# Kernel tuning notes

Hardware: AMD Instinct MI355X
Metric: run time of the kernel (lower is better)

The kernel has to match this reference:

```python
import jax, jax.numpy as jnp
import numpy as np

B, T, V, E, H, K = 64, 1024, 50000, 128, 256, 20
HD = H // 2  # hidden per LSTM direction


def _p(key, i, shape, scale=0.05):
    return jax.random.normal(jax.random.fold_in(key, i), shape, dtype=jnp.float32) * scale


def setup_inputs():
    key = jax.random.key(0)
    k1, k2, k3 = jax.random.split(key, 3)
    lengths = jax.random.randint(k2, (B,), T // 4, T + 1)
    mask = jnp.arange(T)[None, :] < lengths[:, None]  # [B,T] bool, left-aligned
    x = jax.random.randint(k1, (B, T), 1, V)
    x = jnp.where(mask, x, 0).astype(jnp.int32)  # pad_idx = 0
    tags = jax.random.randint(k3, (B, T), 0, K).astype(jnp.int32)
    inp = {"x": x, "tags": tags, "mask": mask}
    pk = jax.random.key(1)
    inp["emb"] = _p(pk, 0, (V, E)).at[0].set(0.0)  # padding_idx row zeroed
    dims = [E, H]  # layer-1 input is concat of both directions = H
    i = 1
    for l in range(2):
        for suf in ["", "_rev"]:
            inp[f"w_ih_l{l}{suf}"] = _p(pk, i, (4 * HD, dims[l])); i += 1
            inp[f"w_hh_l{l}{suf}"] = _p(pk, i, (4 * HD, HD)); i += 1
            inp[f"b_ih_l{l}{suf}"] = _p(pk, i, (4 * HD,)); i += 1
            inp[f"b_hh_l{l}{suf}"] = _p(pk, i, (4 * HD,)); i += 1
    inp["ln_g"] = jnp.ones((H,), jnp.float32)
    inp["ln_b"] = jnp.zeros((H,), jnp.float32)
    inp["attn_w"] = _p(pk, i, (1, H)); i += 1
    inp["attn_b"] = _p(pk, i, (1,)); i += 1
    inp["fc1_w"] = _p(pk, i, (H, H)); i += 1
    inp["fc1_b"] = _p(pk, i, (H,)); i += 1
    inp["fc2_w"] = _p(pk, i, (K, H)); i += 1
    inp["fc2_b"] = _p(pk, i, (K,)); i += 1
    inp["crf_start"] = _p(pk, i, (K,)); i += 1
    inp["crf_end"] = _p(pk, i, (K,)); i += 1
    inp["crf_trans"] = _p(pk, i, (K, K)); i += 1
    return inp


def _lstm_dir(x, w_ih, w_hh, b_ih, b_hh, reverse):
    # x: [B,T,D] -> [B,T,HD]; torch gate order i,f,g,o
    xs = jnp.swapaxes(x, 0, 1)  # [T,B,D]
    pre = xs @ w_ih.T + b_ih + b_hh  # input contribution precomputed (GEMM)

    def step(carry, g_in):
        h, c = carry
        g = g_in + h @ w_hh.T
        i, f, gc, o = jnp.split(g, 4, axis=-1)
        c = jax.nn.sigmoid(f) * c + jax.nn.sigmoid(i) * jnp.tanh(gc)
        h = jax.nn.sigmoid(o) * jnp.tanh(c)
        return (h, c), h

    nB, nH = x.shape[0], w_hh.shape[1]
    init = (jnp.zeros((nB, nH), x.dtype), jnp.zeros((nB, nH), x.dtype))
    _, hs = jax.lax.scan(step, init, pre, reverse=reverse)
    return jnp.swapaxes(hs, 0, 1)


def _crf_nll(emissions, tags, mask, start, end, trans):
    # torchcrf: llh = score - logZ, reduction='sum'; module returns -llh.mean() (scalar)
    maskf = mask.astype(emissions.dtype)
    em_sc = jnp.take_along_axis(emissions, tags[..., None], axis=2)[..., 0]  # [B,T]
    tr_sc = trans[tags[:, :-1], tags[:, 1:]]  # [B,T-1]
    num = start[tags[:, 0]] + em_sc[:, 0] + jnp.sum(maskf[:, 1:] * (tr_sc + em_sc[:, 1:]), axis=1)
    last = jnp.sum(mask.astype(jnp.int32), axis=1) - 1
    last_tags = jnp.take_along_axis(tags, last[:, None], axis=1)[:, 0]
    num = num + end[last_tags]
    alpha0 = start[None, :] + emissions[:, 0]  # [B,K]
    em_t = jnp.swapaxes(emissions[:, 1:], 0, 1)  # [T-1,B,K]
    m_t = jnp.swapaxes(mask[:, 1:], 0, 1)  # [T-1,B]

    def step(alpha, inp):
        e, m = inp
        nxt = jax.scipy.special.logsumexp(alpha[:, :, None] + trans[None] + e[:, None, :], axis=1)
        return jnp.where(m[:, None], nxt, alpha), None

    alpha, _ = jax.lax.scan(step, alpha0, (em_t, m_t))
    logZ = jax.scipy.special.logsumexp(alpha + end[None, :], axis=1)
    return -jnp.sum(num - logZ)


def reference(x, tags, mask, emb,
              w_ih_l0, w_hh_l0, b_ih_l0, b_hh_l0,
              w_ih_l0_rev, w_hh_l0_rev, b_ih_l0_rev, b_hh_l0_rev,
              w_ih_l1, w_hh_l1, b_ih_l1, b_hh_l1,
              w_ih_l1_rev, w_hh_l1_rev, b_ih_l1_rev, b_hh_l1_rev,
              ln_g, ln_b, attn_w, attn_b, fc1_w, fc1_b, fc2_w, fc2_b,
              crf_start, crf_end, crf_trans):
    mask = mask.at[:, 0].set(True)
    h = emb[x]  # [B,T,E]
    # 2-layer bidirectional LSTM (eval mode: dropout = identity)
    h = jnp.concatenate([
        _lstm_dir(h, w_ih_l0, w_hh_l0, b_ih_l0, b_hh_l0, False),
        _lstm_dir(h, w_ih_l0_rev, w_hh_l0_rev, b_ih_l0_rev, b_hh_l0_rev, True)], axis=-1)
    h = jnp.concatenate([
        _lstm_dir(h, w_ih_l1, w_hh_l1, b_ih_l1, b_hh_l1, False),
        _lstm_dir(h, w_ih_l1_rev, w_hh_l1_rev, b_ih_l1_rev, b_hh_l1_rev, True)], axis=-1)
    # LayerNorm (eps=1e-5)
    mu = jnp.mean(h, axis=-1, keepdims=True)
    var = jnp.mean(jnp.square(h - mu), axis=-1, keepdims=True)
    h = (h - mu) * jax.lax.rsqrt(var + 1e-5) * ln_g + ln_b
    # masked attention + residual broadcast of context
    scores = (h @ attn_w.T)[..., 0] + attn_b[0]  # [B,T]
    scores = jnp.where(mask, scores, jnp.float32(-1e9))
    w = jax.nn.softmax(scores, axis=1)[..., None]  # [B,T,1]
    h = h + jnp.sum(h * w, axis=1, keepdims=True)
    # hidden_fc: Linear + ReLU (dropout identity in eval)
    h = jax.nn.relu(h @ fc1_w.T + fc1_b)
    emissions = h @ fc2_w.T + fc2_b  # [B,T,K]
    return _crf_nll(emissions, tags, mask, crf_start, crf_end, crf_trans)
```

## Files before the change

kernel.cpp:

```cpp
#include <hip/hip_runtime.h>
#include <stdint.h>

#define BB 64
#define TT 1024
#define EE 128

typedef __bf16 bf16x8 __attribute__((ext_vector_type(8)));
typedef float f32x4 __attribute__((ext_vector_type(4)));

#define MFMA16 __builtin_amdgcn_mfma_f32_16x16x32_bf16

__device__ __forceinline__ float bf2f(unsigned short u) {
  union { unsigned int i; float f; } v; v.i = ((unsigned int)u) << 16; return v.f;
}
__device__ __forceinline__ unsigned short f2bf(float f) {
  union { float f; unsigned int i; } v; v.f = f;
  return (unsigned short)((v.i + 0x7fffu + ((v.i >> 16) & 1u)) >> 16);
}
__device__ __forceinline__ float sigf(float x) {
  return __builtin_amdgcn_rcpf(1.f + __expf(-x));
}
__device__ __forceinline__ float tanhf_(float x) {
  return fmaf(2.f, __builtin_amdgcn_rcpf(1.f + __expf(-2.f * x)), -1.f);
}


__global__ __launch_bounds__(256) void cvtbf4(const float* __restrict__ s,
                                              unsigned short* __restrict__ d, int n4) {
  int i = blockIdx.x * 256 + threadIdx.x;
  if (i < n4) {
    float4 v = *(const float4*)&s[(size_t)i * 4];
    ushort4 o; o.x = f2bf(v.x); o.y = f2bf(v.y); o.z = f2bf(v.z); o.w = f2bf(v.w);
    *(ushort4*)&d[(size_t)i * 4] = o;
  }
}

__global__ __launch_bounds__(256) void bias_comb(const float* bi, const float* bh,
                                                 const float* bir, const float* bhr,
                                                 float* __restrict__ o) {
  int j = blockIdx.x * 256 + threadIdx.x;
  if (j < 1024) o[j] = (j < 512) ? (bi[j] + bh[j]) : (bir[j - 512] + bhr[j - 512]);
}

__global__ __launch_bounds__(256) void embed_k(const int* __restrict__ x,
                                               const float* __restrict__ emb,
                                               unsigned short* __restrict__ xe) {
  int i = blockIdx.x * 256 + threadIdx.x;
  int bt = i >> 5, e4 = (i & 31) << 2;
  float4 v = *(const float4*)&emb[(size_t)x[bt] * EE + e4];
  ushort4 o; o.x = f2bf(v.x); o.y = f2bf(v.y); o.z = f2bf(v.z); o.w = f2bf(v.w);
  *(ushort4*)&xe[(size_t)bt * EE + e4] = o;
}


template <bool RELU, bool REMAP>
__global__ __launch_bounds__(256) void gemm_bt(const unsigned short* __restrict__ A,
                                               const unsigned short* __restrict__ W,
                                               const float* __restrict__ bias,
                                               unsigned short* __restrict__ out,
                                               int M, int N, int K) {
  __shared__ unsigned short As[64][40];
  __shared__ unsigned short Ws[64][40];
  __shared__ unsigned short Cs[64][72];
  const int tid = threadIdx.x, wave = tid >> 6, lane = tid & 63;
  const int m0 = blockIdx.x * 64, n0 = blockIdx.y * 64;
  f32x4 acc[4] = {{0,0,0,0},{0,0,0,0},{0,0,0,0},{0,0,0,0}};
  const int r = tid >> 2, kc = (tid & 3) << 3;
  const int fr = lane & 15, kk = (lane >> 4) << 3;

  for (int k0 = 0; k0 < K; k0 += 32) {
    uint4 av = *(const uint4*)&A[(size_t)(m0 + r) * K + k0 + kc];
    uint4 wv = *(const uint4*)&W[(size_t)(n0 + r) * K + k0 + kc];
    *(uint4*)&As[r][kc] = av;
    *(uint4*)&Ws[r][kc] = wv;
    __syncthreads();
    bf16x8 af = *(const bf16x8*)&As[wave * 16 + fr][kk];
#pragma unroll
    for (int nt = 0; nt < 4; nt++) {
      bf16x8 bv = *(const bf16x8*)&Ws[nt * 16 + fr][kk];
      acc[nt] = MFMA16(af, bv, acc[nt], 0, 0, 0);
    }
    __syncthreads();
  }
  const int cr = (lane >> 4) << 2, cc = lane & 15;
#pragma unroll
  for (int nt = 0; nt < 4; nt++) {
    float bs = bias[n0 + nt * 16 + cc];
#pragma unroll
    for (int rr = 0; rr < 4; rr++) {
      float v = acc[nt][rr] + bs;
      if (RELU) v = fmaxf(v, 0.f);
      Cs[wave * 16 + cr + rr][nt * 16 + cc] = f2bf(v);
    }
  }
  __syncthreads();
  const int row = tid >> 2, c0 = (tid & 3) * 16;
  uint4 v0 = *(const uint4*)&Cs[row][c0];
  uint4 v1 = *(const uint4*)&Cs[row][c0 + 8];
  const int gm = m0 + row;
  size_t off;
  if (REMAP) { int b = gm >> 10, t = gm & 1023; off = ((size_t)(t * 64 + b)) * N + n0 + c0; }
  else       { off = (size_t)gm * N + n0 + c0; }
  *(uint4*)&out[off] = v0;
  *(uint4*)&out[off + 8] = v1;
}


#define SCAN_STEP10(PG0, PG1, PG2, PG3, TIDX) {                               \
    bf16x8 bv0 = *(const bf16x8*)&hS[p][q * 8];                               \
    bf16x8 bv1 = *(const bf16x8*)&hS[p][32 + q * 8];                          \
    bf16x8 bv2 = *(const bf16x8*)&hS[p][64 + q * 8];                          \
    bf16x8 bv3 = *(const bf16x8*)&hS[p][96 + q * 8];                          \
    f32x4 c0 = {0,0,0,0}, c1 = {0,0,0,0}, c2 = {0,0,0,0}, c3 = {0,0,0,0};     \
    c0 = MFMA16(bv0, af[0][0], c0, 0,0,0); c1 = MFMA16(bv0, af[1][0], c1, 0,0,0); \
    c2 = MFMA16(bv0, af[2][0], c2, 0,0,0); c3 = MFMA16(bv0, af[3][0], c3, 0,0,0); \
    c0 = MFMA16(bv1, af[0][1], c0, 0,0,0); c1 = MFMA16(bv1, af[1][1], c1, 0,0,0); \
    c2 = MFMA16(bv1, af[2][1], c2, 0,0,0); c3 = MFMA16(bv1, af[3][1], c3, 0,0,0); \
    c0 = MFMA16(bv2, af[0][2], c0, 0,0,0); c1 = MFMA16(bv2, af[1][2], c1, 0,0,0); \
    c2 = MFMA16(bv2, af[2][2], c2, 0,0,0); c3 = MFMA16(bv2, af[3][2], c3, 0,0,0); \
    c0 = MFMA16(bv3, af[0][3], c0, 0,0,0); c1 = MFMA16(bv3, af[1][3], c1, 0,0,0); \
    c2 = MFMA16(bv3, af[2][3], c2, 0,0,0); c3 = MFMA16(bv3, af[3][3], c3, 0,0,0); \
    float gi = c0[0] + bf2f(PG0);                                             \
    float gf = c1[0] + bf2f(PG1);                                             \
    float gg = c2[0] + bf2f(PG2);                                             \
    float go = c3[0] + bf2f(PG3);                                             \
    float cn = sigf(gf) * c + sigf(gi) * tanhf_(gg);                          \
    c = cn;                                                                   \
    float h = sigf(go) * tanhf_(cn);                                          \
    unsigned short hb_ = f2bf(h);                                             \
    if (q == 0) {                                                             \
      hS[p ^ 1][u] = hb_;                                                     \
      hob[(size_t)(TIDX) * 256] = hb_;                   \
    }                                                                         \
  }

__global__ __launch_bounds__(512) void lstm_scan10(const unsigned short* __restrict__ pre,
                                                   const unsigned short* __restrict__ whhb,
                                                   unsigned short* __restrict__ hout) {
  const int b = blockIdx.x, dir = blockIdx.y;
  const int tid = threadIdx.x;
  const int w = tid >> 6, lane = tid & 63;
  const int fr = lane & 15, q = lane >> 4;
  const int u = 16 * w + fr;
  const unsigned short* wb = whhb + (size_t)dir * 65536;

  bf16x8 af[4][4];
#pragma unroll
  for (int G = 0; G < 4; G++)
#pragma unroll
    for (int kt = 0; kt < 4; kt++)
      af[G][kt] = *(const bf16x8*)&wb[(size_t)(128 * G + 16 * w + fr) * 128 + kt * 32 + q * 8];
  asm volatile("" : "+v"(af[0][0]), "+v"(af[0][1]), "+v"(af[0][2]), "+v"(af[0][3]),
                    "+v"(af[1][0]), "+v"(af[1][1]), "+v"(af[1][2]), "+v"(af[1][3]),
                    "+v"(af[2][0]), "+v"(af[2][1]), "+v"(af[2][2]), "+v"(af[2][3]),
                    "+v"(af[3][0]), "+v"(af[3][1]), "+v"(af[3][2]), "+v"(af[3][3]));

  __shared__ alignas(16) unsigned short hS[2][128];
  if (tid < 128) { hS[0][tid] = 0; hS[1][tid] = 0; }

  const int t0 = dir ? 1023 : 0, st = dir ? -1 : 1;
  float c = 0.f;
  const unsigned short* pb = pre + (size_t)b * 1024 + dir * 512 + u;
  unsigned short* hob = hout + (size_t)b * 1024 * 256 + dir * 128 + u;

  unsigned short pA0, pA1, pA2, pA3, pB0, pB1, pB2, pB3;
  {
    size_t tb = (size_t)t0 * 65536;
    pA0 = pb[tb]; pA1 = pb[tb + 128]; pA2 = pb[tb + 256]; pA3 = pb[tb + 384];
    tb = (size_t)(t0 + st) * 65536;
    pB0 = pb[tb]; pB1 = pb[tb + 128]; pB2 = pb[tb + 256]; pB3 = pb[tb + 384];
  }
  __syncthreads();

  int p = 0;
  for (int s = 0; s < 1024; s += 2) {
    const int t = t0 + st * s;
    SCAN_STEP10(pA0, pA1, pA2, pA3, t)
    if (s + 2 < 1024) {
      size_t tb = (size_t)(t0 + st * (s + 2)) * 65536;
      pA0 = pb[tb]; pA1 = pb[tb + 128]; pA2 = pb[tb + 256]; pA3 = pb[tb + 384];
    }
    asm volatile("s_waitcnt lgkmcnt(0)\n\ts_barrier" ::: "memory");
    p ^= 1;
    SCAN_STEP10(pB0, pB1, pB2, pB3, t + st)
    if (s + 3 < 1024) {
      size_t tb = (size_t)(t0 + st * (s + 3)) * 65536;
      pB0 = pb[tb]; pB1 = pb[tb + 128]; pB2 = pb[tb + 256]; pB3 = pb[tb + 384];
    }
    asm volatile("s_waitcnt lgkmcnt(0)\n\ts_barrier" ::: "memory");
    p ^= 1;
  }
}


__global__ __launch_bounds__(256) void ln_attn(const unsigned short* __restrict__ h,
                                               const float* __restrict__ g,
                                               const float* __restrict__ be,
                                               const float* __restrict__ aw,
                                               const float* __restrict__ ab,
                                               unsigned short* __restrict__ hln,
                                               float* __restrict__ sc) {
  int row = blockIdx.x * 4 + (threadIdx.x >> 6);
  int lane = threadIdx.x & 63;
  ushort4 u = *(const ushort4*)&h[(size_t)row * 256 + lane * 4];
  float vx = bf2f(u.x), vy = bf2f(u.y), vz = bf2f(u.z), vw = bf2f(u.w);
  float s = vx + vy + vz + vw;
#pragma unroll
  for (int o = 1; o < 64; o <<= 1) s += __shfl_xor(s, o);
  float mu = s * (1.f / 256.f);
  float dx = vx - mu, dy = vy - mu, dz = vz - mu, dw = vw - mu;
  float q = dx * dx + dy * dy + dz * dz + dw * dw;
#pragma unroll
  for (int o = 1; o < 64; o <<= 1) q += __shfl_xor(q, o);
  float inv = rsqrtf(q * (1.f / 256.f) + 1e-5f);
  float4 gg = *(const float4*)&g[lane * 4];
  float4 bb = *(const float4*)&be[lane * 4];
  float y0 = dx * inv * gg.x + bb.x;
  float y1 = dy * inv * gg.y + bb.y;
  float y2 = dz * inv * gg.z + bb.z;
  float y3 = dw * inv * gg.w + bb.w;
  ushort4 ov; ov.x = f2bf(y0); ov.y = f2bf(y1); ov.z = f2bf(y2); ov.w = f2bf(y3);
  *(ushort4*)&hln[(size_t)row * 256 + lane * 4] = ov;
  float4 av = *(const float4*)&aw[lane * 4];
  float p = y0 * av.x + y1 * av.y + y2 * av.z + y3 * av.w;
#pragma unroll
  for (int o = 1; o < 64; o <<= 1) p += __shfl_xor(p, o);
  if (lane == 0) sc[row] = p + ab[0];
}


__global__ __launch_bounds__(256) void attn_pool(const float* __restrict__ scores,
                                                 const int* __restrict__ x,
                                                 const unsigned short* __restrict__ h_ln,
                                                 float* __restrict__ pooled) {
  int b = blockIdx.x, tid = threadIdx.x;
  __shared__ float wls[1024];
  __shared__ float red[4];
  float mx = -1e30f;
  for (int t = tid; t < 1024; t += 256) {
    bool valid = (t == 0) || (x[b * 1024 + t] != 0);
    float s = valid ? scores[b * 1024 + t] : -1e9f;
    wls[t] = s;
    mx = fmaxf(mx, s);
  }
#pragma unroll
  for (int o = 1; o < 64; o <<= 1) mx = fmaxf(mx, __shfl_xor(mx, o));
  if ((tid & 63) == 0) red[tid >> 6] = mx;
  __syncthreads();
  mx = fmaxf(fmaxf(red[0], red[1]), fmaxf(red[2], red[3]));
  __syncthreads();
  float sm = 0.f;
  for (int t = tid; t < 1024; t += 256) {
    float e = __expf(wls[t] - mx);
    wls[t] = e;
    sm += e;
  }
#pragma unroll
  for (int o = 1; o < 64; o <<= 1) sm += __shfl_xor(sm, o);
  if ((tid & 63) == 0) red[tid >> 6] = sm;
  __syncthreads();
  sm = red[0] + red[1] + red[2] + red[3];
  float inv = 1.f / sm;
  float a0 = 0.f, a1 = 0.f, a2 = 0.f, a3 = 0.f;
  const unsigned short* hb = h_ln + (size_t)b * 1024 * 256 + tid;
  for (int t = 0; t < 1024; t += 4) {
    a0 = fmaf(wls[t + 0], bf2f(hb[(size_t)(t + 0) * 256]), a0);
    a1 = fmaf(wls[t + 1], bf2f(hb[(size_t)(t + 1) * 256]), a1);
    a2 = fmaf(wls[t + 2], bf2f(hb[(size_t)(t + 2) * 256]), a2);
    a3 = fmaf(wls[t + 3], bf2f(hb[(size_t)(t + 3) * 256]), a3);
  }
  pooled[b * 256 + tid] = ((a0 + a1) + (a2 + a3)) * inv;
}

__global__ __launch_bounds__(256) void h2add(const unsigned short* __restrict__ h_ln,
                                             const float* __restrict__ pooled,
                                             unsigned short* __restrict__ h2) {
  size_t i = ((size_t)blockIdx.x * 256 + threadIdx.x) * 4;
  int b = (int)(i >> 18);
  int cidx = (int)(i & 255);
  ushort4 v = *(const ushort4*)&h_ln[i];
  float4 p = *(const float4*)&pooled[b * 256 + cidx];
  ushort4 o;
  o.x = f2bf(bf2f(v.x) + p.x); o.y = f2bf(bf2f(v.y) + p.y);
  o.z = f2bf(bf2f(v.z) + p.z); o.w = f2bf(bf2f(v.w) + p.w);
  *(ushort4*)&h2[i] = o;
}


__global__ __launch_bounds__(256) void fc2_emis(const unsigned short* __restrict__ fin,
                                                const float* __restrict__ w,
                                                const float* __restrict__ bias,
                                                float* __restrict__ em) {
  int row = blockIdx.x * 4 + (threadIdx.x >> 6);
  int lane = threadIdx.x & 63;
  ushort4 u = *(const ushort4*)&fin[(size_t)row * 256 + lane * 4];
  float x0 = bf2f(u.x), x1 = bf2f(u.y), x2 = bf2f(u.z), x3 = bf2f(u.w);
  float acc[20];
#pragma unroll
  for (int jj = 0; jj < 20; jj++) {
    float4 wv = *(const float4*)&w[jj * 256 + lane * 4];
    acc[jj] = x0 * wv.x + x1 * wv.y + x2 * wv.z + x3 * wv.w;
  }
#pragma unroll
  for (int jj = 0; jj < 20; jj++) {
#pragma unroll
    for (int o = 1; o < 64; o <<= 1) acc[jj] += __shfl_xor(acc[jj], o);
  }
  if (lane == 0) {
#pragma unroll
    for (int jj = 0; jj < 20; jj++) em[(size_t)row * 20 + jj] = acc[jj] + bias[jj];
  }
}


__global__ __launch_bounds__(64) void crf_k(const float* __restrict__ em,
                                            const int* __restrict__ tags,
                                            const int* __restrict__ x,
                                            const float* __restrict__ cs,
                                            const float* __restrict__ ce,
                                            const float* __restrict__ ctr,
                                            float* __restrict__ part) {
  int b = blockIdx.x, lane = threadIdx.x;
  const float* eb = em + (size_t)b * 1024 * 20;
  const int* tb = tags + b * 1024;
  const int* xb = x + b * 1024;

  int cnt = 0;
  for (int t = lane; t < 1024; t += 64) cnt += (t == 0 || xb[t] != 0) ? 1 : 0;
#pragma unroll
  for (int o = 1; o < 64; o <<= 1) cnt += __shfl_xor(cnt, o);
  int len = cnt;

  float ns = 0.f;
  for (int t = 1 + lane; t < len; t += 64)
    ns += ctr[tb[t - 1] * 20 + tb[t]] + eb[(size_t)t * 20 + tb[t]];
#pragma unroll
  for (int o = 1; o < 64; o <<= 1) ns += __shfl_xor(ns, o);
  float num = ns + cs[tb[0]] + eb[tb[0]] + ce[tb[len - 1]];

  __shared__ float al[32];
  if (lane < 32) al[lane] = (lane < 20) ? (cs[lane] + eb[lane]) : -1e30f;
  __syncthreads();

  int p = lane / 20, jj = lane % 20;
  int i0 = p * 7;
  float trc[7];
#pragma unroll
  for (int i = 0; i < 7; i++)
    trc[i] = (i0 + i < 20) ? ctr[(i0 + i) * 20 + jj] : -1e30f;

  for (int t = 1; t < len; t++) {
    float aa[7];
    float m = -3e30f;
#pragma unroll
    for (int i = 0; i < 7; i++) {
      float a = ((i0 + i < 28) ? al[i0 + i] : -1e30f) + trc[i];
      aa[i] = a;
      m = fmaxf(m, a);
    }
    float m0 = __shfl(m, jj), m1 = __shfl(m, jj + 20), m2 = __shfl(m, jj + 40);
    float mj = fmaxf(fmaxf(m0, m1), m2);
    float s = 0.f;
#pragma unroll
    for (int i = 0; i < 7; i++) s += __expf(aa[i] - mj);
    float s0 = __shfl(s, jj), s1 = __shfl(s, jj + 20), s2 = __shfl(s, jj + 40);
    float na = mj + __logf(s0 + s1 + s2) + eb[(size_t)t * 20 + jj];
    __syncthreads();
    if (lane < 20) al[lane] = na;
    __syncthreads();
  }

  float v = (lane < 20) ? (al[lane] + ce[lane]) : -3e30f;
  float mm = v;
#pragma unroll
  for (int o = 1; o < 64; o <<= 1) mm = fmaxf(mm, __shfl_xor(mm, o));
  float ss = (lane < 20) ? __expf(v - mm) : 0.f;
#pragma unroll
  for (int o = 1; o < 64; o <<= 1) ss += __shfl_xor(ss, o);
  float logZ = mm + __logf(ss);
  if (lane == 0) part[b] = logZ - num;
}

__global__ __launch_bounds__(64) void finalsum(const float* __restrict__ part,
                                               float* __restrict__ out) {
  float v = part[threadIdx.x];
#pragma unroll
  for (int o = 1; o < 64; o <<= 1) v += __shfl_xor(v, o);
  if (threadIdx.x == 0) out[0] = v;
}


extern "C" void kernel_launch(void* const* d_in, const int* in_sizes, int n_in,
                              void* d_out, int out_size, void* d_ws, size_t ws_size,
                              hipStream_t stream) {
  (void)in_sizes; (void)n_in; (void)out_size; (void)ws_size;
  const int*   x     = (const int*)  d_in[0];
  const int*   tags  = (const int*)  d_in[1];
  const float* emb   = (const float*)d_in[3];
  const float* wih0  = (const float*)d_in[4];
  const float* whh0  = (const float*)d_in[5];
  const float* bih0  = (const float*)d_in[6];
  const float* bhh0  = (const float*)d_in[7];
  const float* wih0r = (const float*)d_in[8];
  const float* whh0r = (const float*)d_in[9];
  const float* bih0r = (const float*)d_in[10];
  const float* bhh0r = (const float*)d_in[11];
  const float* wih1  = (const float*)d_in[12];
  const float* whh1  = (const float*)d_in[13];
  const float* bih1  = (const float*)d_in[14];
  const float* bhh1  = (const float*)d_in[15];
  const float* wih1r = (const float*)d_in[16];
  const float* whh1r = (const float*)d_in[17];
  const float* bih1r = (const float*)d_in[18];
  const float* bhh1r = (const float*)d_in[19];
  const float* lng   = (const float*)d_in[20];
  const float* lnb   = (const float*)d_in[21];
  const float* attw  = (const float*)d_in[22];
  const float* attb  = (const float*)d_in[23];
  const float* fc1w  = (const float*)d_in[24];
  const float* fc1b  = (const float*)d_in[25];
  const float* fc2w  = (const float*)d_in[26];
  const float* fc2b  = (const float*)d_in[27];
  const float* cst   = (const float*)d_in[28];
  const float* cen   = (const float*)d_in[29];
  const float* ctr   = (const float*)d_in[30];

  char* base = (char*)d_ws;
  const size_t MB = 1024 * 1024;

  unsigned short* PRE  = (unsigned short*)(base);
  unsigned short* HLN  = (unsigned short*)(base);
  unsigned short* H2   = (unsigned short*)(base + 64 * MB);
  unsigned short* FC1O = (unsigned short*)(base + 96 * MB);
  unsigned short* XEMB = (unsigned short*)(base + 128 * MB);
  unsigned short* HL0  = (unsigned short*)(base + 128 * MB);
  unsigned short* HL1  = (unsigned short*)(base + 128 * MB);
  float*          EM   = (float*)(base + 128 * MB);
  char* sm = base + 160 * MB;
  unsigned short* WIH0  = (unsigned short*)sm;  sm += (size_t)2 * 512 * 128 * 2;
  unsigned short* WIH1  = (unsigned short*)sm;  sm += (size_t)2 * 512 * 256 * 2;
  unsigned short* FC1W  = (unsigned short*)sm;  sm += (size_t)256 * 256 * 2;
  unsigned short* WHHB0 = (unsigned short*)sm;  sm += (size_t)2 * 512 * 128 * 2;
  unsigned short* WHHB1 = (unsigned short*)sm;  sm += (size_t)2 * 512 * 128 * 2;
  float* BIAS0 = (float*)sm; sm += 1024 * 4;
  float* BIAS1 = (float*)sm; sm += 1024 * 4;
  float* SCORE = (float*)sm; sm += (size_t)BB * TT * 4;
  float* POOL  = (float*)sm; sm += 64 * 256 * 4;
  float* PART  = (float*)sm; sm += 256;

  cvtbf4<<<64, 256, 0, stream>>>(wih0, WIH0, 65536 / 4);
  cvtbf4<<<64, 256, 0, stream>>>(wih0r, WIH0 + 65536, 65536 / 4);
  cvtbf4<<<128, 256, 0, stream>>>(wih1, WIH1, 131072 / 4);
  cvtbf4<<<128, 256, 0, stream>>>(wih1r, WIH1 + 131072, 131072 / 4);
  cvtbf4<<<64, 256, 0, stream>>>(fc1w, FC1W, 65536 / 4);
  cvtbf4<<<64, 256, 0, stream>>>(whh0, WHHB0, 65536 / 4);
  cvtbf4<<<64, 256, 0, stream>>>(whh0r, WHHB0 + 65536, 65536 / 4);
  cvtbf4<<<64, 256, 0, stream>>>(whh1, WHHB1, 65536 / 4);
  cvtbf4<<<64, 256, 0, stream>>>(whh1r, WHHB1 + 65536, 65536 / 4);
  bias_comb<<<4, 256, 0, stream>>>(bih0, bhh0, bih0r, bhh0r, BIAS0);
  bias_comb<<<4, 256, 0, stream>>>(bih1, bhh1, bih1r, bhh1r, BIAS1);

  embed_k<<<8192, 256, 0, stream>>>(x, emb, XEMB);

  gemm_bt<false, true><<<dim3(1024, 16), 256, 0, stream>>>(XEMB, WIH0, BIAS0, PRE, 65536, 1024, 128);
  lstm_scan10<<<dim3(64, 2), 512, 0, stream>>>(PRE, WHHB0, HL0);

  gemm_bt<false, true><<<dim3(1024, 16), 256, 0, stream>>>(HL0, WIH1, BIAS1, PRE, 65536, 1024, 256);
  lstm_scan10<<<dim3(64, 2), 512, 0, stream>>>(PRE, WHHB1, HL1);

  ln_attn<<<16384, 256, 0, stream>>>(HL1, lng, lnb, attw, attb, HLN, SCORE);
  attn_pool<<<64, 256, 0, stream>>>(SCORE, x, HLN, POOL);
  h2add<<<16384, 256, 0, stream>>>(HLN, POOL, H2);

  gemm_bt<true, false><<<dim3(1024, 4), 256, 0, stream>>>(H2, FC1W, fc1b, FC1O, 65536, 256, 256);
  fc2_emis<<<16384, 256, 0, stream>>>(FC1O, fc2w, fc2b, EM);

  crf_k<<<64, 64, 0, stream>>>(EM, tags, x, cst, cen, ctr, PART);
  finalsum<<<1, 64, 0, stream>>>(PART, (float*)d_out);
}
```

Before: 1.709 ms.

## Use 128x128 GEMM tiles, merge weight conversions, fuse pooling residual add

The projection GEMMs now use 128x128 output tiles with a K-step of 64. Each wave computes a 4x4 grid of MFMA tiles, so each operand fragment is reused more and fewer blocks are launched. The nine weight-conversion launches are merged into one kernel that picks its source range by index. The separate h2add kernel is folded into the attention-pooling kernel, which drops the pooled buffer and a launch, but now only 64 blocks stream the whole hidden tensor.

```diff
diff --git a/kernel.cpp b/kernel.cpp
--- a/kernel.cpp
+++ b/kernel.cpp
@@ -25,14 +25,30 @@
 }
 
 
-__global__ __launch_bounds__(256) void cvtbf4(const float* __restrict__ s,
-                                              unsigned short* __restrict__ d, int n4) {
+__global__ __launch_bounds__(256) void cvt_all(const float* s0, unsigned short* d0,
+                                               const float* s1, unsigned short* d1,
+                                               const float* s2, unsigned short* d2,
+                                               const float* s3, unsigned short* d3,
+                                               const float* s4, unsigned short* d4,
+                                               const float* s5, unsigned short* d5,
+                                               const float* s6, unsigned short* d6,
+                                               const float* s7, unsigned short* d7,
+                                               const float* s8, unsigned short* d8) {
   int i = blockIdx.x * 256 + threadIdx.x;
-  if (i < n4) {
-    float4 v = *(const float4*)&s[(size_t)i * 4];
-    ushort4 o; o.x = f2bf(v.x); o.y = f2bf(v.y); o.z = f2bf(v.z); o.w = f2bf(v.w);
-    *(ushort4*)&d[(size_t)i * 4] = o;
-  }
+  const float* s; unsigned short* d; int off;
+  if      (i <  16384) { s = s0; d = d0; off = 0; }
+  else if (i <  32768) { s = s1; d = d1; off = 16384; }
+  else if (i <  65536) { s = s2; d = d2; off = 32768; }
+  else if (i <  98304) { s = s3; d = d3; off = 65536; }
+  else if (i < 114688) { s = s4; d = d4; off = 98304; }
+  else if (i < 131072) { s = s5; d = d5; off = 114688; }
+  else if (i < 147456) { s = s6; d = d6; off = 131072; }
+  else if (i < 163840) { s = s7; d = d7; off = 147456; }
+  else                 { s = s8; d = d8; off = 163840; }
+  int k = i - off;
+  float4 v = *(const float4*)&s[(size_t)k * 4];
+  ushort4 o; o.x = f2bf(v.x); o.y = f2bf(v.y); o.z = f2bf(v.z); o.w = f2bf(v.w);
+  *(ushort4*)&d[(size_t)k * 4] = o;
 }
 
 __global__ __launch_bounds__(256) void bias_comb(const float* bi, const float* bh,
@@ -54,55 +70,77 @@
 
 
 template <bool RELU, bool REMAP>
-__global__ __launch_bounds__(256) void gemm_bt(const unsigned short* __restrict__ A,
+__global__ __launch_bounds__(256) void gemm128(const unsigned short* __restrict__ A,
                                                const unsigned short* __restrict__ W,
                                                const float* __restrict__ bias,
                                                unsigned short* __restrict__ out,
                                                int M, int N, int K) {
-  __shared__ unsigned short As[64][40];
-  __shared__ unsigned short Ws[64][40];
-  __shared__ unsigned short Cs[64][72];
+  __shared__ unsigned short LB[2 * 128 * 72];
   const int tid = threadIdx.x, wave = tid >> 6, lane = tid & 63;
-  const int m0 = blockIdx.x * 64, n0 = blockIdx.y * 64;
-  f32x4 acc[4] = {{0,0,0,0},{0,0,0,0},{0,0,0,0},{0,0,0,0}};
-  const int r = tid >> 2, kc = (tid & 3) << 3;
-  const int fr = lane & 15, kk = (lane >> 4) << 3;
-
-  for (int k0 = 0; k0 < K; k0 += 32) {
-    uint4 av = *(const uint4*)&A[(size_t)(m0 + r) * K + k0 + kc];
-    uint4 wv = *(const uint4*)&W[(size_t)(n0 + r) * K + k0 + kc];
-    *(uint4*)&As[r][kc] = av;
-    *(uint4*)&Ws[r][kc] = wv;
+  const int fr = lane & 15, q = lane >> 4;
+  const int m0 = blockIdx.x * 128, n0 = blockIdx.y * 128;
+  const int wm = (wave & 1) * 64, wn = (wave >> 1) * 64;
+  f32x4 acc[4][4] = {};
+  const int sr = tid >> 1, sc = (tid & 1) * 32;
+
+  for (int k0 = 0; k0 < K; k0 += 64) {
+    const unsigned short* ga = &A[(size_t)(m0 + sr) * K + k0 + sc];
+    const unsigned short* gw = &W[(size_t)(n0 + sr) * K + k0 + sc];
+    uint4 a0 = *(const uint4*)&ga[0],  a1 = *(const uint4*)&ga[8];
+    uint4 a2 = *(const uint4*)&ga[16], a3 = *(const uint4*)&ga[24];
+    uint4 w0 = *(const uint4*)&gw[0],  w1 = *(const uint4*)&gw[8];
+    uint4 w2 = *(const uint4*)&gw[16], w3 = *(const uint4*)&gw[24];
     __syncthreads();
-    bf16x8 af = *(const bf16x8*)&As[wave * 16 + fr][kk];
-#pragma unroll
-    for (int nt = 0; nt < 4; nt++) {
-      bf16x8 bv = *(const bf16x8*)&Ws[nt * 16 + fr][kk];
-      acc[nt] = MFMA16(af, bv, acc[nt], 0, 0, 0);
+    *(uint4*)&LB[sr * 72 + sc +  0] = a0;
+    *(uint4*)&LB[sr * 72 + sc +  8] = a1;
+    *(uint4*)&LB[sr * 72 + sc + 16] = a2;
+    *(uint4*)&LB[sr * 72 + sc + 24] = a3;
+    *(uint4*)&LB[9216 + sr * 72 + sc +  0] = w0;
+    *(uint4*)&LB[9216 + sr * 72 + sc +  8] = w1;
+    *(uint4*)&LB[9216 + sr * 72 + sc + 16] = w2;
+    *(uint4*)&LB[9216 + sr * 72 + sc + 24] = w3;
+    __syncthreads();
+#pragma unroll
+    for (int kt = 0; kt < 2; kt++) {
+      bf16x8 afr[4], bfr[4];
+#pragma unroll
+      for (int i = 0; i < 4; i++)
+        afr[i] = *(const bf16x8*)&LB[(wm + i * 16 + fr) * 72 + kt * 32 + q * 8];
+#pragma unroll
+      for (int j = 0; j < 4; j++)
+        bfr[j] = *(const bf16x8*)&LB[9216 + (wn + j * 16 + fr) * 72 + kt * 32 + q * 8];
+#pragma unroll
+      for (int i = 0; i < 4; i++)
+#pragma unroll
+        for (int j = 0; j < 4; j++)
+          acc[i][j] = MFMA16(afr[i], bfr[j], acc[i][j], 0, 0, 0);
     }
-    __syncthreads();
-  }
-  const int cr = (lane >> 4) << 2, cc = lane & 15;
-#pragma unroll
-  for (int nt = 0; nt < 4; nt++) {
-    float bs = bias[n0 + nt * 16 + cc];
-#pragma unroll
-    for (int rr = 0; rr < 4; rr++) {
-      float v = acc[nt][rr] + bs;
-      if (RELU) v = fmaxf(v, 0.f);
-      Cs[wave * 16 + cr + rr][nt * 16 + cc] = f2bf(v);
-    }
-  }
-  __syncthreads();
-  const int row = tid >> 2, c0 = (tid & 3) * 16;
-  uint4 v0 = *(const uint4*)&Cs[row][c0];
-  uint4 v1 = *(const uint4*)&Cs[row][c0 + 8];
+  }
+  __syncthreads();
+  const int cc = fr, cr = q * 4;
+#pragma unroll
+  for (int j = 0; j < 4; j++) {
+    float bs = bias[n0 + wn + j * 16 + cc];
+#pragma unroll
+    for (int i = 0; i < 4; i++)
+#pragma unroll
+      for (int rr = 0; rr < 4; rr++) {
+        float v = acc[i][j][rr] + bs;
+        if (RELU) v = fmaxf(v, 0.f);
+        LB[(wm + i * 16 + cr + rr) * 136 + wn + j * 16 + cc] = f2bf(v);
+      }
+  }
+  __syncthreads();
+  const int row = tid >> 1, hf = (tid & 1) * 64;
   const int gm = m0 + row;
   size_t off;
-  if (REMAP) { int b = gm >> 10, t = gm & 1023; off = ((size_t)(t * 64 + b)) * N + n0 + c0; }
-  else       { off = (size_t)gm * N + n0 + c0; }
-  *(uint4*)&out[off] = v0;
-  *(uint4*)&out[off + 8] = v1;
+  if (REMAP) { int b = gm >> 10, t = gm & 1023; off = ((size_t)(t * 64 + b)) * N + n0 + hf; }
+  else       { off = (size_t)gm * N + n0 + hf; }
+#pragma unroll
+  for (int j = 0; j < 8; j++) {
+    uint4 v = *(const uint4*)&LB[row * 136 + hf + j * 8];
+    *(uint4*)&out[off + j * 8] = v;
+  }
 }
 
 
@@ -229,10 +267,10 @@
 }
 
 
-__global__ __launch_bounds__(256) void attn_pool(const float* __restrict__ scores,
-                                                 const int* __restrict__ x,
-                                                 const unsigned short* __restrict__ h_ln,
-                                                 float* __restrict__ pooled) {
+__global__ __launch_bounds__(256) void attn_pool_h2(const float* __restrict__ scores,
+                                                    const int* __restrict__ x,
+                                                    const unsigned short* __restrict__ h_ln,
+                                                    unsigned short* __restrict__ h2) {
   int b = blockIdx.x, tid = threadIdx.x;
   __shared__ float wls[1024];
   __shared__ float red[4];
@@ -269,21 +307,11 @@
     a2 = fmaf(wls[t + 2], bf2f(hb[(size_t)(t + 2) * 256]), a2);
     a3 = fmaf(wls[t + 3], bf2f(hb[(size_t)(t + 3) * 256]), a3);
   }
-  pooled[b * 256 + tid] = ((a0 + a1) + (a2 + a3)) * inv;
-}
-
-__global__ __launch_bounds__(256) void h2add(const unsigned short* __restrict__ h_ln,
-                                             const float* __restrict__ pooled,
-                                             unsigned short* __restrict__ h2) {
-  size_t i = ((size_t)blockIdx.x * 256 + threadIdx.x) * 4;
-  int b = (int)(i >> 18);
-  int cidx = (int)(i & 255);
-  ushort4 v = *(const ushort4*)&h_ln[i];
-  float4 p = *(const float4*)&pooled[b * 256 + cidx];
-  ushort4 o;
-  o.x = f2bf(bf2f(v.x) + p.x); o.y = f2bf(bf2f(v.y) + p.y);
-  o.z = f2bf(bf2f(v.z) + p.z); o.w = f2bf(bf2f(v.w) + p.w);
-  *(ushort4*)&h2[i] = o;
+  float pooled = ((a0 + a1) + (a2 + a3)) * inv;
+  unsigned short* ob = h2 + (size_t)b * 1024 * 256 + tid;
+#pragma unroll 4
+  for (int t = 0; t < 1024; t++)
+    ob[(size_t)t * 256] = f2bf(bf2f(hb[(size_t)t * 256]) + pooled);
 }
 
 
@@ -445,34 +473,32 @@
   float* BIAS0 = (float*)sm; sm += 1024 * 4;
   float* BIAS1 = (float*)sm; sm += 1024 * 4;
   float* SCORE = (float*)sm; sm += (size_t)BB * TT * 4;
-  float* POOL  = (float*)sm; sm += 64 * 256 * 4;
   float* PART  = (float*)sm; sm += 256;
 
-  cvtbf4<<<64, 256, 0, stream>>>(wih0, WIH0, 65536 / 4);
-  cvtbf4<<<64, 256, 0, stream>>>(wih0r, WIH0 + 65536, 65536 / 4);
-  cvtbf4<<<128, 256, 0, stream>>>(wih1, WIH1, 131072 / 4);
-  cvtbf4<<<128, 256, 0, stream>>>(wih1r, WIH1 + 131072, 131072 / 4);
-  cvtbf4<<<64, 256, 0, stream>>>(fc1w, FC1W, 65536 / 4);
-  cvtbf4<<<64, 256, 0, stream>>>(whh0, WHHB0, 65536 / 4);
-  cvtbf4<<<64, 256, 0, stream>>>(whh0r, WHHB0 + 65536, 65536 / 4);
-  cvtbf4<<<64, 256, 0, stream>>>(whh1, WHHB1, 65536 / 4);
-  cvtbf4<<<64, 256, 0, stream>>>(whh1r, WHHB1 + 65536, 65536 / 4);
+  cvt_all<<<704, 256, 0, stream>>>(wih0, WIH0,
+                                   wih0r, WIH0 + 65536,
+                                   wih1, WIH1,
+                                   wih1r, WIH1 + 131072,
+                                   fc1w, FC1W,
+                                   whh0, WHHB0,
+                                   whh0r, WHHB0 + 65536,
+                                   whh1, WHHB1,
+                                   whh1r, WHHB1 + 65536);
   bias_comb<<<4, 256, 0, stream>>>(bih0, bhh0, bih0r, bhh0r, BIAS0);
   bias_comb<<<4, 256, 0, stream>>>(bih1, bhh1, bih1r, bhh1r, BIAS1);
 
   embed_k<<<8192, 256, 0, stream>>>(x, emb, XEMB);
 
-  gemm_bt<false, true><<<dim3(1024, 16), 256, 0, stream>>>(XEMB, WIH0, BIAS0, PRE, 65536, 1024, 128);
+  gemm128<false, true><<<dim3(512, 8), 256, 0, stream>>>(XEMB, WIH0, BIAS0, PRE, 65536, 1024, 128);
   lstm_scan10<<<dim3(64, 2), 512, 0, stream>>>(PRE, WHHB0, HL0);
 
-  gemm_bt<false, true><<<dim3(1024, 16), 256, 0, stream>>>(HL0, WIH1, BIAS1, PRE, 65536, 1024, 256);
+  gemm128<false, true><<<dim3(512, 8), 256, 0, stream>>>(HL0, WIH1, BIAS1, PRE, 65536, 1024, 256);
   lstm_scan10<<<dim3(64, 2), 512, 0, stream>>>(PRE, WHHB1, HL1);
 
   ln_attn<<<16384, 256, 0, stream>>>(HL1, lng, lnb, attw, attb, HLN, SCORE);
-  attn_pool<<<64, 256, 0, stream>>>(SCORE, x, HLN, POOL);
-  h2add<<<16384, 256, 0, stream>>>(HLN, POOL, H2);
-
-  gemm_bt<true, false><<<dim3(1024, 4), 256, 0, stream>>>(H2, FC1W, fc1b, FC1O, 65536, 256, 256);
+  attn_pool_h2<<<64, 256, 0, stream>>>(SCORE, x, HLN, H2);
+
+  gemm128<true, false><<<dim3(512, 2), 256, 0, stream>>>(H2, FC1W, fc1b, FC1O, 65536, 256, 256);
   fc2_emis<<<16384, 256, 0, stream>>>(FC1O, fc2w, fc2b, EM);
 
   crf_k<<<64, 64, 0, stream>>>(EM, tags, x, cst, cen, ctr, PART);
```

After: 1.733 ms. No clear change (+1.4%).
